# Performance work log

Measured on AMD Instinct MI355X. Metric: run time of the kernel, lower is better.

Reference implementation:

```python
import jax, jax.numpy as jnp
import numpy as np

DEFOCUS_MAX = 4.0
R_MAX = int(DEFOCUS_MAX) + 1   # matches kernel's intRadius = int(fltRadius) + 1 at max defocus
GAMMA = 4.0                    # tanh sharpness of the soft disk edge
PI = 3.141592653589793


def setup_inputs():
    key = jax.random.key(0)
    k1, k2 = jax.random.split(key)
    B, C, H, W = 2, 3, 512, 512
    image = jax.random.uniform(k1, (B, C, H, W), dtype=jnp.float32)
    # signed per-pixel circle-of-confusion radius, scaled to [0, DEFOCUS_MAX)
    defocus = jax.random.uniform(k2, (B, 1, H, W), dtype=jnp.float32) * DEFOCUS_MAX
    return {"image": image, "defocus": defocus}


def _render(image, defocus):
    # Scatter form (CUDA kernel): every source pixel p splats w(p, dist) * image[p]
    # into all q with |q-p|_inf <= int(|defocus[p]|)+1, plus w into weight_cum.
    # Equivalent gather form used here: out[q] = sum over offsets o of
    # w(q-o, |o|) * image[q-o], vectorized over all pixels per offset.
    B, C, H, W = image.shape
    R = R_MAX
    r = jnp.abs(defocus)                              # CoC radius per source pixel
    int_r = jnp.floor(r) + 1.0                        # square scatter window half-size
    inv_area = 1.0 / jnp.maximum(PI * r * r, 1.0)     # disk-area normalization

    pad = ((0, 0), (0, 0), (R, R), (R, R))
    img_p = jnp.pad(image, pad)
    r_p = jnp.pad(r, pad)
    ir_p = jnp.pad(int_r, pad)
    inv_p = jnp.pad(inv_area, pad)
    val_p = jnp.pad(jnp.ones((B, 1, H, W), jnp.float32), pad)  # in-bounds source mask

    offs = np.stack(np.meshgrid(np.arange(-R, R + 1), np.arange(-R, R + 1),
                                indexing='ij'), -1).reshape(-1, 2)
    offs = jnp.asarray(offs, jnp.int32)               # ((2R+1)^2, 2)

    def body(carry, off):
        bokeh, wsum = carry
        dy, dx = off[0], off[1]
        y0, x0 = R - dy, R - dx                       # source p = q - (dy, dx)
        src_img = jax.lax.dynamic_slice(img_p, (0, 0, y0, x0), (B, C, H, W))
        src_r = jax.lax.dynamic_slice(r_p, (0, 0, y0, x0), (B, 1, H, W))
        src_ir = jax.lax.dynamic_slice(ir_p, (0, 0, y0, x0), (B, 1, H, W))
        src_inv = jax.lax.dynamic_slice(inv_p, (0, 0, y0, x0), (B, 1, H, W))
        src_val = jax.lax.dynamic_slice(val_p, (0, 0, y0, x0), (B, 1, H, W))
        dist = jnp.sqrt((dy * dy + dx * dx).astype(jnp.float32))
        in_win = (jnp.abs(dy).astype(jnp.float32) <= src_ir) & \
                 (jnp.abs(dx).astype(jnp.float32) <= src_ir)
        w = (0.5 + 0.5 * jnp.tanh(GAMMA * (src_r - dist))) * src_inv
        w = jnp.where(in_win, w, 0.0) * src_val
        return (bokeh + w * src_img, wsum + w), None

    init = (jnp.zeros((B, C, H, W), jnp.float32),
            jnp.zeros((B, 1, H, W), jnp.float32))
    (bokeh_cum, weight_cum), _ = jax.lax.scan(jax.checkpoint(body), init, offs)
    return bokeh_cum / weight_cum


def reference(image, defocus):
    return _render(image, defocus)
```

## Files before the change

### kernel.cpp

```cpp
#include <hip/hip_runtime.h>
#include <cmath>


#define HH 512
#define WW 512
#define NB 2
#define TW 64
#define TH 32
#define HALO 4
#define SROWS (TH + 2 * HALO)
#define LW 72

__device__ __forceinline__ unsigned rtne_hi(float v) {
  unsigned u = __float_as_uint(v);
  u = u + 0x7FFFu + ((u >> 16) & 1u);
  return u & 0xFFFF0000u;
}

__global__ __launch_bounds__(512, 2) void bokeh_gather(
    const float* __restrict__ img,
    const float* __restrict__ def,
    float* __restrict__ out)
{
  __shared__ __align__(16) unsigned sX[SROWS][LW];
  __shared__ __align__(16) unsigned sY[SROWS][LW];
  __shared__ __align__(16) unsigned sZ[SROWS][LW];
  __shared__ float sFd[9][12];

  const int tid = threadIdx.x;
  const int tx  = tid & 15;
  const int ty  = tid >> 4;
  const int bx = blockIdx.x * TW;
  const int by = blockIdx.y * TH;
  const int b  = blockIdx.z;

  if (tid < 81) {
    int dyi = tid / 9, dxi = tid - dyi * 9;
    int dyo = dyi - 4, dxo = dxi - 4;
    float d2 = (float)(dyo * dyo + dxo * dxo);
    sFd[dyi][dxi] = __expf(8.0f * sqrtf(d2));
  }

  const float* dpt = def + b * (HH * WW);
  const float* ipt = img + b * (3 * HH * WW);

  for (int idx = tid; idx < SROWS * LW; idx += 512) {
    int ly = idx / LW;
    int lx = idx - ly * LW;
    int sy = by - HALO + ly;
    int sx = bx - HALO + lx;
    unsigned X = 0u, Y = 0u, Z = 0u;
    if (sy >= 0 && sy < HH && sx >= 0 && sx < WW) {
      int o = sy * WW + sx;
      float r = fabsf(dpt[o]);
      float G  = __expf(-8.0f * r);
      float iv = __builtin_amdgcn_rcpf(fmaxf(3.14159265358979f * r * r, 1.0f));
      X = rtne_hi(G) | (rtne_hi(iv) >> 16);
      Y = rtne_hi(ipt[o]) | (rtne_hi(ipt[o + HH * WW]) >> 16);
      Z = rtne_hi(ipt[o + 2 * HH * WW]);
    }
    sX[ly][lx] = X;
    sY[ly][lx] = Y;
    sZ[ly][lx] = Z;
  }
  __syncthreads();

  float wsum[4] = {0.f, 0.f, 0.f, 0.f};
  float ac0[4]  = {0.f, 0.f, 0.f, 0.f};
  float ac1[4]  = {0.f, 0.f, 0.f, 0.f};
  float ac2[4]  = {0.f, 0.f, 0.f, 0.f};

  const int col0 = 4 * tx;

  #pragma unroll 1
  for (int dy = 0; dy < 9; ++dy) {
    const int sr = ty + dy;
    float fdr[9];
    #pragma unroll
    for (int x = 0; x < 9; ++x) fdr[x] = sFd[dy][x];

    unsigned Xv[12], Yv[12], Zv[12];
    #pragma unroll
    for (int q = 0; q < 3; ++q) {
      *(uint4*)&Xv[4 * q] = *(const uint4*)(&sX[sr][col0] + 4 * q);
      *(uint4*)&Yv[4 * q] = *(const uint4*)(&sY[sr][col0] + 4 * q);
      *(uint4*)&Zv[4 * q] = *(const uint4*)(&sZ[sr][col0] + 4 * q);
    }
    float Gv[12], Iv[12], C0[12], C1[12];
    #pragma unroll
    for (int j = 0; j < 12; ++j) {
      Gv[j] = __uint_as_float(Xv[j] & 0xFFFF0000u);
      Iv[j] = __uint_as_float(Xv[j] << 16);
      C0[j] = __uint_as_float(Yv[j] & 0xFFFF0000u);
      C1[j] = __uint_as_float(Yv[j] << 16);
    }

    #pragma unroll
    for (int k = 0; k < 4; ++k) {
      #pragma unroll
      for (int j = k; j < k + 9; ++j) {
        const int xi = j - k;
        float tden = fmaf(Gv[j], fdr[xi], 1.0f);
        float w = __builtin_amdgcn_rcpf(tden) * Iv[j];
        wsum[k] += w;
        ac0[k] = fmaf(w, C0[j], ac0[k]);
        ac1[k] = fmaf(w, C1[j], ac1[k]);
        ac2[k] = fmaf(w, __uint_as_float(Zv[j]), ac2[k]);
      }
    }
  }

  const int oy = by + ty;
  const int ox = bx + col0;
  float rw[4];
  #pragma unroll
  for (int k = 0; k < 4; ++k) rw[k] = __builtin_amdgcn_rcpf(wsum[k]);

  float* op0 = out + ((b * 3 + 0) * HH + oy) * WW + ox;
  float* op1 = out + ((b * 3 + 1) * HH + oy) * WW + ox;
  float* op2 = out + ((b * 3 + 2) * HH + oy) * WW + ox;
  float4 v0, v1, v2;
  v0.x = ac0[0] * rw[0]; v0.y = ac0[1] * rw[1]; v0.z = ac0[2] * rw[2]; v0.w = ac0[3] * rw[3];
  v1.x = ac1[0] * rw[0]; v1.y = ac1[1] * rw[1]; v1.z = ac1[2] * rw[2]; v1.w = ac1[3] * rw[3];
  v2.x = ac2[0] * rw[0]; v2.y = ac2[1] * rw[1]; v2.z = ac2[2] * rw[2]; v2.w = ac2[3] * rw[3];
  *(float4*)op0 = v0;
  *(float4*)op1 = v1;
  *(float4*)op2 = v2;
}

extern "C" void kernel_launch(void* const* d_in, const int* in_sizes, int n_in,
                              void* d_out, int out_size, void* d_ws, size_t ws_size,
                              hipStream_t stream) {
  const float* img = (const float*)d_in[0];
  const float* def = (const float*)d_in[1];
  float* out = (float*)d_out;

  dim3 grid(WW / TW, HH / TH, NB);
  dim3 block(512);
  hipLaunchKernelGGL(bokeh_gather, grid, block, 0, stream, img, def, out);
}
```

Baseline: 20.60 us.

## Split stencil rows across two thread halves with shared-memory reduction, halve tile height

Tile height drops from 32 to 16 rows. The two 256-thread halves of each block now split the 9 vertical offsets (5 rows and 4 rows), and their partial sums are combined through a shared-memory buffer before the divide and store. Launch bounds now target 4 blocks per CU, and the third channel is truncated instead of round-to-nearest when packed to bf16. The aim is more blocks and better latency hiding for the 512x512 problem. The cost is a larger halo fraction per tile, an extra barrier and reduction, an imbalanced 5/4 split, and tighter register limits.

```diff
diff --git a/kernel.cpp b/kernel.cpp
--- a/kernel.cpp
+++ b/kernel.cpp
@@ -6,7 +6,7 @@
 #define WW 512
 #define NB 2
 #define TW 64
-#define TH 32
+#define TH 16
 #define HALO 4
 #define SROWS (TH + 2 * HALO)
 #define LW 72
@@ -17,7 +17,7 @@
   return u & 0xFFFF0000u;
 }
 
-__global__ __launch_bounds__(512, 2) void bokeh_gather(
+__global__ __launch_bounds__(512, 4) void bokeh_gather(
     const float* __restrict__ img,
     const float* __restrict__ def,
     float* __restrict__ out)
@@ -26,10 +26,13 @@
   __shared__ __align__(16) unsigned sY[SROWS][LW];
   __shared__ __align__(16) unsigned sZ[SROWS][LW];
   __shared__ float sFd[9][12];
+  __shared__ __align__(16) float pbuf[256][20];
 
   const int tid = threadIdx.x;
-  const int tx  = tid & 15;
-  const int ty  = tid >> 4;
+  const int s   = tid >> 8;
+  const int t   = tid & 255;
+  const int tx  = t & 15;
+  const int ty  = t >> 4;
   const int bx = blockIdx.x * TW;
   const int by = blockIdx.y * TH;
   const int b  = blockIdx.z;
@@ -50,14 +53,14 @@
     int sy = by - HALO + ly;
     int sx = bx - HALO + lx;
     unsigned X = 0u, Y = 0u, Z = 0u;
-    if (sy >= 0 && sy < HH && sx >= 0 && sx < WW) {
+    if ((unsigned)sy < (unsigned)HH && (unsigned)sx < (unsigned)WW) {
       int o = sy * WW + sx;
       float r = fabsf(dpt[o]);
       float G  = __expf(-8.0f * r);
       float iv = __builtin_amdgcn_rcpf(fmaxf(3.14159265358979f * r * r, 1.0f));
       X = rtne_hi(G) | (rtne_hi(iv) >> 16);
       Y = rtne_hi(ipt[o]) | (rtne_hi(ipt[o + HH * WW]) >> 16);
-      Z = rtne_hi(ipt[o + 2 * HH * WW]);
+      Z = __float_as_uint(ipt[o + 2 * HH * WW]) & 0xFFFF0000u;
     }
     sX[ly][lx] = X;
     sY[ly][lx] = Y;
@@ -71,9 +74,11 @@
   float ac2[4]  = {0.f, 0.f, 0.f, 0.f};
 
   const int col0 = 4 * tx;
+  const int dy0 = s ? 5 : 0;
+  const int dy1 = s ? 9 : 5;
 
   #pragma unroll 1
-  for (int dy = 0; dy < 9; ++dy) {
+  for (int dy = dy0; dy < dy1; ++dy) {
     const int sr = ty + dy;
     float fdr[9];
     #pragma unroll
@@ -110,22 +115,44 @@
     }
   }
 
-  const int oy = by + ty;
-  const int ox = bx + col0;
-  float rw[4];
-  #pragma unroll
-  for (int k = 0; k < 4; ++k) rw[k] = __builtin_amdgcn_rcpf(wsum[k]);
+  if (s == 1) {
+    float4 v0 = {wsum[0], wsum[1], wsum[2], wsum[3]};
+    float4 v1 = {ac0[0], ac0[1], ac0[2], ac0[3]};
+    float4 v2 = {ac1[0], ac1[1], ac1[2], ac1[3]};
+    float4 v3 = {ac2[0], ac2[1], ac2[2], ac2[3]};
+    *(float4*)&pbuf[t][0]  = v0;
+    *(float4*)&pbuf[t][4]  = v1;
+    *(float4*)&pbuf[t][8]  = v2;
+    *(float4*)&pbuf[t][12] = v3;
+  }
+  __syncthreads();
+  if (s == 0) {
+    float4 v0 = *(const float4*)&pbuf[t][0];
+    float4 v1 = *(const float4*)&pbuf[t][4];
+    float4 v2 = *(const float4*)&pbuf[t][8];
+    float4 v3 = *(const float4*)&pbuf[t][12];
+    wsum[0] += v0.x; wsum[1] += v0.y; wsum[2] += v0.z; wsum[3] += v0.w;
+    ac0[0] += v1.x; ac0[1] += v1.y; ac0[2] += v1.z; ac0[3] += v1.w;
+    ac1[0] += v2.x; ac1[1] += v2.y; ac1[2] += v2.z; ac1[3] += v2.w;
+    ac2[0] += v3.x; ac2[1] += v3.y; ac2[2] += v3.z; ac2[3] += v3.w;
 
-  float* op0 = out + ((b * 3 + 0) * HH + oy) * WW + ox;
-  float* op1 = out + ((b * 3 + 1) * HH + oy) * WW + ox;
-  float* op2 = out + ((b * 3 + 2) * HH + oy) * WW + ox;
-  float4 v0, v1, v2;
-  v0.x = ac0[0] * rw[0]; v0.y = ac0[1] * rw[1]; v0.z = ac0[2] * rw[2]; v0.w = ac0[3] * rw[3];
-  v1.x = ac1[0] * rw[0]; v1.y = ac1[1] * rw[1]; v1.z = ac1[2] * rw[2]; v1.w = ac1[3] * rw[3];
-  v2.x = ac2[0] * rw[0]; v2.y = ac2[1] * rw[1]; v2.z = ac2[2] * rw[2]; v2.w = ac2[3] * rw[3];
-  *(float4*)op0 = v0;
-  *(float4*)op1 = v1;
-  *(float4*)op2 = v2;
+    const int oy = by + ty;
+    const int ox = bx + col0;
+    float rw[4];
+    #pragma unroll
+    for (int k = 0; k < 4; ++k) rw[k] = __builtin_amdgcn_rcpf(wsum[k]);
+
+    float* op0 = out + ((b * 3 + 0) * HH + oy) * WW + ox;
+    float* op1 = out + ((b * 3 + 1) * HH + oy) * WW + ox;
+    float* op2 = out + ((b * 3 + 2) * HH + oy) * WW + ox;
+    float4 o0, o1, o2;
+    o0.x = ac0[0] * rw[0]; o0.y = ac0[1] * rw[1]; o0.z = ac0[2] * rw[2]; o0.w = ac0[3] * rw[3];
+    o1.x = ac1[0] * rw[0]; o1.y = ac1[1] * rw[1]; o1.z = ac1[2] * rw[2]; o1.w = ac1[3] * rw[3];
+    o2.x = ac2[0] * rw[0]; o2.y = ac2[1] * rw[1]; o2.z = ac2[2] * rw[2]; o2.w = ac2[3] * rw[3];
+    *(float4*)op0 = o0;
+    *(float4*)op1 = o1;
+    *(float4*)op2 = o2;
+  }
 }
 
 extern "C" void kernel_launch(void* const* d_in, const int* in_sizes, int n_in,
```

New measurement: 19.36 us. 6.0% less time.
